# Kernel optimization log

Hardware: AMD Instinct MI355X
Metric: run time of the kernel (lower is better)

The kernel has to match this reference:

```python
import jax, jax.numpy as jnp
import numpy as np

N, E, IN_DIM, OUT_DIM, NTYPE, QDIM = 32, 512, 300, 300, 4, 300
SLOPE = 0.2  # lrelu:0.2


def setup_inputs() -> dict:
    key = jax.random.key(0)
    ks = jax.random.split(key, 8)
    return {
        "input_state": jax.random.normal(ks[0], (N, E, IN_DIM), jnp.float32),
        "adj": jax.random.randint(ks[1], (N, E, E), 0, NTYPE + 1, dtype=jnp.int32),
        "node_mask": jax.random.uniform(ks[2], (N, E, 1), jnp.float32),
        "query_vec": jax.random.normal(ks[3], (N, QDIM), jnp.float32),
        "W_type": jax.random.normal(ks[4], (NTYPE, IN_DIM, OUT_DIM), jnp.float32) * 0.02,
        "a_type": jax.random.normal(ks[5], (NTYPE, 2 * OUT_DIM), jnp.float32) * 0.02,
        "qattn_W1": jax.random.normal(ks[6], (NTYPE, QDIM, 2 * OUT_DIM), jnp.float32) * 0.02,
        "qattn_W2": jax.random.normal(ks[7], (NTYPE, 2 * OUT_DIM, 2 * OUT_DIM), jnp.float32) * 0.02,
    }


def reference(input_state, adj, node_mask, query_vec, W_type, a_type, qattn_W1, qattn_W2):
    # Faithful GAT head. The original builds an [N,E,E,2d] concat tensor; since
    # a_input[n,i,j] = [h_i, h_j] and the gate broadcasts over (i,j), the score
    # decomposes exactly as lrelu((h*g1)@a1 [:,i,None] + (h*g2)@a2 [:,None,j]).
    lrelu = lambda x: jnp.where(x >= 0, x, SLOPE * x)
    scores = jnp.zeros(adj.shape, jnp.float32)
    h = None
    for i in range(NTYPE):
        h = jnp.einsum("ned,df->nef", input_state, W_type[i])  # [N,E,d] (dropout: eval no-op)
        q_gate = jax.nn.relu(query_vec @ qattn_W1[i])
        q_gate = jax.nn.sigmoid(q_gate @ qattn_W2[i])          # [N,2d]
        g1, g2 = q_gate[:, :OUT_DIM], q_gate[:, OUT_DIM:]
        a1, a2 = a_type[i][:OUT_DIM], a_type[i][OUT_DIM:]
        s_src = jnp.einsum("ned,d->ne", h * g1[:, None, :], a1)  # contributes along i
        s_dst = jnp.einsum("ned,d->ne", h * g2[:, None, :], a2)  # contributes along j
        score = lrelu(s_src[:, :, None] + s_dst[:, None, :])      # [N,E,E]
        scores = scores + jnp.where(adj == i + 1, score, 0.0)
    scores = jnp.where(adj > 0, scores, jnp.float32(-1e30))
    h = h * node_mask  # note: original applies mask to h from the LAST edge type
    coefs = jax.nn.softmax(scores, axis=2)
    return jnp.einsum("nij,njd->nid", coefs, h)
```

## Files before the change

kernel.cpp:

```cpp
#include <hip/hip_runtime.h>
#include <hip/hip_bf16.h>

#define Nn   32
#define Ee   512
#define DIN  300
#define DOUT 300
#define NT   4
#define QD   300
#define SLOPE 0.2f
#define ROWS 64
#define CPAD 320
#define SSTR 516
#define USTR 65

typedef __attribute__((ext_vector_type(8))) short bf16x8;
typedef __attribute__((ext_vector_type(4))) float f32x4;
typedef __attribute__((ext_vector_type(4))) unsigned short u16x4;

__device__ inline unsigned short f2bf(float x) {
    __hip_bfloat16 h = __float2bfloat16(x);
    return *reinterpret_cast<unsigned short*>(&h);
}
__device__ inline float bf2f(unsigned short u) {
    __hip_bfloat16 h = *reinterpret_cast<__hip_bfloat16*>(&u);
    return __bfloat162float(h);
}
__device__ inline int swzj(int j) { return j ^ ((j >> 5) & 3); }

__global__ __launch_bounds__(256) void prep_kernel(
    const float* __restrict__ W3,
    unsigned short* __restrict__ W3T_hi,
    unsigned short* __restrict__ W3T_lo,
    unsigned short* __restrict__ UTh,
    unsigned short* __restrict__ UTl,
    unsigned short* __restrict__ GTh,
    unsigned short* __restrict__ GTl)
{
    int idx = blockIdx.x * 256 + threadIdx.x;
    if (idx < 320 * 320) {
        int c = idx / 320, k = idx - c * 320;
        float v = (c < DOUT && k < DIN) ? W3[(size_t)k * DOUT + c] : 0.f;
        unsigned short h = f2bf(v);
        W3T_hi[idx] = h;
        W3T_lo[idx] = f2bf(v - bf2f(h));
    }
    if (idx < 32 * 16 * 320) { UTh[idx] = 0; UTl[idx] = 0; }
    if (idx < 4 * 64 * 320)  { GTh[idx] = 0; GTl[idx] = 0; }
}

__global__ __launch_bounds__(256) void gates1_part_kernel(
    const float* __restrict__ q,
    const float* __restrict__ W1,
    float* __restrict__ t1p)
{
    int i = blockIdx.y, z = blockIdx.z;
    int idx = blockIdx.x * 256 + threadIdx.x;
    int n = idx / 600, j = idx - n * 600;
    const float* W1i = W1 + (size_t)i * QD * 600;
    const float* qn = q + n * QD;
    int k0 = z * 75;
    float a0 = 0.f;
    #pragma unroll 5
    for (int k = k0; k < k0 + 75; ++k)
        a0 += qn[k] * W1i[(size_t)k * 600 + j];
    t1p[((size_t)(z * NT + i) * Nn + n) * 600 + j] = a0;
}

__global__ __launch_bounds__(256) void gates1_fin_kernel(
    const float* __restrict__ t1p, float* __restrict__ t1)
{
    int i = blockIdx.y;
    int idx = blockIdx.x * 256 + threadIdx.x;
    size_t o = ((size_t)i * Nn) * 600 + idx;
    float s = t1p[o] + t1p[o + 76800] + t1p[o + 2 * 76800] + t1p[o + 3 * 76800];
    t1[o] = fmaxf(s, 0.f);
}

__global__ __launch_bounds__(256) void gates2_part_kernel(
    const float* __restrict__ t1,
    const float* __restrict__ W2,
    float* __restrict__ gp)
{
    int i = blockIdx.y, z = blockIdx.z;
    int idx = blockIdx.x * 256 + threadIdx.x;
    int n = idx / 600, j = idx - n * 600;
    const float* W2i = W2 + (size_t)i * 600 * 600;
    const float* tn = t1 + ((size_t)i * Nn + n) * 600;
    int k0 = z * 150;
    float a0 = 0.f, a1 = 0.f;
    #pragma unroll 5
    for (int k = k0; k < k0 + 150; k += 2) {
        a0 += tn[k]     * W2i[(size_t)k * 600 + j];
        a1 += tn[k + 1] * W2i[(size_t)(k + 1) * 600 + j];
    }
    gp[((size_t)(z * NT + i) * Nn + n) * 600 + j] = a0 + a1;
}

__global__ __launch_bounds__(256) void gates2_fin_kernel(
    const float* __restrict__ gp,
    const float* __restrict__ a,
    unsigned short* __restrict__ GTh,
    unsigned short* __restrict__ GTl)
{
    int i = blockIdx.y;
    int idx = blockIdx.x * 256 + threadIdx.x;
    int n = idx / 600, j = idx - n * 600;
    size_t o = ((size_t)i * Nn + n) * 600 + j;
    float s = gp[o] + gp[o + 76800] + gp[o + 2 * 76800] + gp[o + 3 * 76800];
    float w = (1.f / (1.f + __expf(-s))) * a[(size_t)i * 600 + j];
    int s2 = (j >= DOUT) ? 1 : 0;
    int d = j - s2 * DOUT;
    int c = 2 * n + s2;
    size_t go = ((size_t)i * 64 + c) * 320 + d;
    unsigned short h = f2bf(w);
    GTh[go] = h;
    GTl[go] = f2bf(w - bf2f(h));
}

__global__ __launch_bounds__(256) void uvec_mfma_kernel(
    const float* __restrict__ W,
    const unsigned short* __restrict__ GTh,
    const unsigned short* __restrict__ GTl,
    unsigned short* __restrict__ UTh,
    unsigned short* __restrict__ UTl)
{
    int mc = blockIdx.x, i = blockIdx.y;
    int tid = threadIdx.x, wv = tid >> 6, lane = tid & 63;
    int g = lane >> 4, cr = lane & 15;
    int m0 = mc * 64 + wv * 16;
    int arow = m0 + cr;
    const float* wr = W + (size_t)i * DIN * DOUT
                        + (size_t)(arow < DIN ? arow : 0) * DOUT;

    f32x4 acc[4];
    #pragma unroll
    for (int nt = 0; nt < 4; ++nt) acc[nt] = (f32x4){0.f, 0.f, 0.f, 0.f};

    for (int ks = 0; ks < 10; ++ks) {
        int k0 = ks * 32 + 8 * g;
        float x8[8];
        if (ks < 9) {
            f32x4 v0 = *(const f32x4*)(wr + k0);
            f32x4 v1 = *(const f32x4*)(wr + k0 + 4);
            #pragma unroll
            for (int j = 0; j < 4; ++j) { x8[j] = v0[j]; x8[4 + j] = v1[j]; }
        } else {
            #pragma unroll
            for (int j = 0; j < 8; ++j) {
                int d = k0 + j;
                x8[j] = (d < DOUT) ? wr[d] : 0.f;
            }
        }
        bf16x8 ahi, alo;
        #pragma unroll
        for (int j = 0; j < 8; ++j) {
            unsigned short h = f2bf(x8[j]);
            ahi[j] = (short)h;
            alo[j] = (short)f2bf(x8[j] - bf2f(h));
        }
        #pragma unroll
        for (int nt = 0; nt < 4; ++nt) {
            size_t bo = ((size_t)i * 64 + nt * 16 + cr) * 320 + k0;
            bf16x8 bh = *(const bf16x8*)(GTh + bo);
            bf16x8 bl = *(const bf16x8*)(GTl + bo);
            acc[nt] = __builtin_amdgcn_mfma_f32_16x16x32_bf16(ahi, bh, acc[nt], 0, 0, 0);
            acc[nt] = __builtin_amdgcn_mfma_f32_16x16x32_bf16(ahi, bl, acc[nt], 0, 0, 0);
            acc[nt] = __builtin_amdgcn_mfma_f32_16x16x32_bf16(alo, bh, acc[nt], 0, 0, 0);
        }
    }

    int krow = m0 + 4 * g;
    if (krow < DIN) {
        #pragma unroll
        for (int nt = 0; nt < 4; ++nt) {
            int c = nt * 16 + cr;
            int n = c >> 1, s = c & 1;
            size_t base = ((size_t)n * 16 + 2 * i + s) * 320 + krow;
            u16x4 h4, l4;
            #pragma unroll
            for (int q = 0; q < 4; ++q) {
                float v = acc[nt][q];
                unsigned short h = f2bf(v);
                h4[q] = h;
                l4[q] = f2bf(v - bf2f(h));
            }
            *(u16x4*)(UTh + base) = h4;
            *(u16x4*)(UTl + base) = l4;
        }
    }
}

__global__ __launch_bounds__(512) void hm_mfma_kernel(
    const float* __restrict__ X,
    const float* __restrict__ mask,
    const unsigned short* __restrict__ W3T_hi,
    const unsigned short* __restrict__ W3T_lo,
    const unsigned short* __restrict__ UTh,
    const unsigned short* __restrict__ UTl,
    unsigned short* __restrict__ hmT_hi,
    unsigned short* __restrict__ hmT_lo,
    float* __restrict__ ssrc,
    float* __restrict__ sdst)
{
    int tid = threadIdx.x, wv = tid >> 6, lane = tid & 63;
    int g = lane >> 4, cr = lane & 15;
    int f  = blockIdx.x;
    int n  = (f & 7) * 4 + ((f >> 3) & 3);
    int j0 = (f >> 5) * 64;
    size_t row0 = (size_t)n * Ee + j0;

    __shared__ float maskL[64];
    if (tid < 64) maskL[tid] = mask[row0 + tid];
    __syncthreads();

    f32x4 acc[3][4];
    f32x4 sacc[4];
    #pragma unroll
    for (int t = 0; t < 3; ++t)
        #pragma unroll
        for (int m = 0; m < 4; ++m) acc[t][m] = (f32x4){0.f, 0.f, 0.f, 0.f};
    #pragma unroll
    for (int m = 0; m < 4; ++m) sacc[m] = (f32x4){0.f, 0.f, 0.f, 0.f};

    const float* xr0 = X + (row0 +      cr) * DIN;
    const float* xr1 = X + (row0 + 16 + cr) * DIN;
    const float* xr2 = X + (row0 + 32 + cr) * DIN;
    const float* xr3 = X + (row0 + 48 + cr) * DIN;
    const float* xrs[4] = {xr0, xr1, xr2, xr3};

    for (int ks = 0; ks < 10; ++ks) {
        int k0 = ks * 32 + 8 * g;
        bf16x8 ahi[4], alo[4];
        #pragma unroll
        for (int m = 0; m < 4; ++m) {
            const float* xr = xrs[m];
            float x8[8];
            if (ks < 9) {
                f32x4 v0 = *(const f32x4*)(xr + k0);
                f32x4 v1 = *(const f32x4*)(xr + k0 + 4);
                #pragma unroll
                for (int j = 0; j < 4; ++j) { x8[j] = v0[j]; x8[4 + j] = v1[j]; }
            } else {
                #pragma unroll
                for (int j = 0; j < 8; ++j) {
                    int k = k0 + j;
                    x8[j] = (k < DIN) ? xr[k] : 0.f;
                }
            }
            #pragma unroll
            for (int j = 0; j < 8; ++j) {
                unsigned short h = f2bf(x8[j]);
                ahi[m][j] = (short)h;
                alo[m][j] = (short)f2bf(x8[j] - bf2f(h));
            }
        }
        #pragma unroll
        for (int t = 0; t < 3; ++t) {
            int ct = wv + 8 * t;
            if (ct < 19) {
                int c = ct * 16 + cr;
                bf16x8 bh = *(const bf16x8*)(W3T_hi + (size_t)c * 320 + k0);
                bf16x8 bl = *(const bf16x8*)(W3T_lo + (size_t)c * 320 + k0);
                #pragma unroll
                for (int m = 0; m < 4; ++m) {
                    acc[t][m] = __builtin_amdgcn_mfma_f32_16x16x32_bf16(ahi[m], bh, acc[t][m], 0, 0, 0);
                    acc[t][m] = __builtin_amdgcn_mfma_f32_16x16x32_bf16(ahi[m], bl, acc[t][m], 0, 0, 0);
                    acc[t][m] = __builtin_amdgcn_mfma_f32_16x16x32_bf16(alo[m], bh, acc[t][m], 0, 0, 0);
                }
            }
        }
        if (wv == 0) {
            bf16x8 uh = *(const bf16x8*)(UTh + ((size_t)n * 16 + cr) * 320 + k0);
            bf16x8 ul = *(const bf16x8*)(UTl + ((size_t)n * 16 + cr) * 320 + k0);
            #pragma unroll
            for (int m = 0; m < 4; ++m) {
                sacc[m] = __builtin_amdgcn_mfma_f32_16x16x32_bf16(ahi[m], uh, sacc[m], 0, 0, 0);
                sacc[m] = __builtin_amdgcn_mfma_f32_16x16x32_bf16(ahi[m], ul, sacc[m], 0, 0, 0);
                sacc[m] = __builtin_amdgcn_mfma_f32_16x16x32_bf16(alo[m], uh, sacc[m], 0, 0, 0);
            }
        }
    }

    #pragma unroll
    for (int t = 0; t < 3; ++t) {
        int ct = wv + 8 * t;
        if (ct < 19) {
            int c = ct * 16 + cr;
            #pragma unroll
            for (int m = 0; m < 4; ++m) {
                u16x4 h4, l4;
                #pragma unroll
                for (int qq = 0; qq < 4; ++qq) {
                    float v = acc[t][m][qq] * maskL[m * 16 + 4 * g + qq];
                    unsigned short h = f2bf(v);
                    h4[qq] = h;
                    l4[qq] = f2bf(v - bf2f(h));
                }
                size_t off = ((size_t)(n * CPAD + c)) * Ee + j0 + m * 16 + 4 * g;
                *(u16x4*)(hmT_hi + off) = h4;
                *(u16x4*)(hmT_lo + off) = l4;
            }
        }
    }

    if (wv == 0 && cr < 8) {
        int i = cr >> 1;
        float* dst = (cr & 1) ? sdst : ssrc;
        #pragma unroll
        for (int m = 0; m < 4; ++m)
            #pragma unroll
            for (int qq = 0; qq < 4; ++qq)
                dst[((size_t)i * Nn + n) * Ee + j0 + m * 16 + 4 * g + qq] = sacc[m][qq];
    }
}

__global__ __launch_bounds__(1024, 1) void attn64_kernel(
    const int*   __restrict__ adj,
    const float* __restrict__ ssrc,
    const float* __restrict__ sdst,
    const unsigned short* __restrict__ hmT_hi,
    const unsigned short* __restrict__ hmT_lo,
    float* __restrict__ out)
{
    int f  = blockIdx.x;
    int n  = (f & 7) * 4 + ((f >> 3) & 3);
    int rt = f >> 5;
    int tid = threadIdx.x;
    int row0 = rt * ROWS;

    __shared__ unsigned uni[Ee * USTR];
    __shared__ float sdl[NT * Ee];
    __shared__ float ssl[NT * 65];
    float* S = (float*)uni;

    for (int idx = tid; idx < NT * Ee; idx += 1024) {
        int i = idx >> 9, j = idx & (Ee - 1);
        sdl[i * Ee + swzj(j)] = sdst[((size_t)i * Nn + n) * Ee + j];
    }
    if (tid < NT * ROWS) {
        int i = tid >> 6, r = tid & 63;
        ssl[i * 65 + r] = ssrc[((size_t)i * Nn + n) * Ee + row0 + r];
    }
    __syncthreads();

    const int* adjb = adj + ((size_t)n * Ee + row0) * Ee;
    for (int idx4 = tid; idx4 < (ROWS * Ee) / 4; idx4 += 1024) {
        int r  = idx4 >> 7;
        int jb = (idx4 & 127) << 2;
        int xw = (jb >> 5) & 3;
        int4 t4 = *(const int4*)(adjb + (idx4 << 2));
        int tv[4] = {t4.x, t4.y, t4.z, t4.w};
        f32x4 v4;
        #pragma unroll
        for (int u = 0; u < 4; ++u) {
            int t = tv[u];
            float v;
            if (t > 0) {
                float x = ssl[(t - 1) * 65 + r] + sdl[(t - 1) * Ee + jb + (u ^ xw)];
                v = (x >= 0.f) ? x : SLOPE * x;
            } else {
                v = -1e30f;
            }
            v4[u] = v;
        }
        *(f32x4*)(S + r * SSTR + jb) = v4;
    }
    __syncthreads();

    int wv = tid >> 6, lane = tid & 63;
    float vals[4][8];
    float inv[4];
    #pragma unroll
    for (int rr = 0; rr < 4; ++rr) {
        int r = wv * 4 + rr;
        float m = -3.0e38f;
        #pragma unroll
        for (int k = 0; k < 8; ++k) {
            vals[rr][k] = S[r * SSTR + lane + 64 * k];
            m = fmaxf(m, vals[rr][k]);
        }
        #pragma unroll
        for (int off = 32; off; off >>= 1) m = fmaxf(m, __shfl_xor(m, off));
        float s = 0.f;
        #pragma unroll
        for (int k = 0; k < 8; ++k) {
            vals[rr][k] = __expf(vals[rr][k] - m);
            s += vals[rr][k];
        }
        #pragma unroll
        for (int off = 32; off; off >>= 1) s += __shfl_xor(s, off);
        inv[rr] = 1.f / s;
    }
    __syncthreads();

    #pragma unroll
    for (int rr = 0; rr < 4; ++rr) {
        int r = wv * 4 + rr;
        #pragma unroll
        for (int k = 0; k < 8; ++k) {
            float v = vals[rr][k] * inv[rr];
            unsigned short hi = f2bf(v);
            unsigned short lo = f2bf(v - bf2f(hi));
            uni[(lane + 64 * k) * USTR + r] = ((unsigned)hi << 16) | (unsigned)lo;
        }
    }
    __syncthreads();

    int g = lane >> 4, cr = lane & 15;
    f32x4 acc[2][4];
    #pragma unroll
    for (int t = 0; t < 2; ++t)
        #pragma unroll
        for (int m = 0; m < 4; ++m) acc[t][m] = (f32x4){0.f, 0.f, 0.f, 0.f};

#define LOADB(BH, BL, KS) do {                                              \
    int kk_ = (KS) * 32 + 8 * g;                                            \
    _Pragma("unroll")                                                       \
    for (int t_ = 0; t_ < 2; ++t_) {                                        \
        int ct_ = wv + 16 * t_;                                             \
        if (ct_ < 19) {                                                     \
            size_t off_ = ((size_t)(n * CPAD + ct_ * 16 + cr)) * Ee + kk_;  \
            BH[t_] = *(const bf16x8*)(hmT_hi + off_);                       \
            BL[t_] = *(const bf16x8*)(hmT_lo + off_);                       \
        }                                                                   \
    }                                                                       \
} while (0)

#define PVSTEP(KS, BH, BL) do {                                             \
    int kk_ = (KS) * 32;                                                    \
    bf16x8 ahi_[4], alo_[4];                                                \
    _Pragma("unroll")                                                       \
    for (int m_ = 0; m_ < 4; ++m_) {                                        \
        _Pragma("unroll")                                                   \
        for (int j_ = 0; j_ < 8; ++j_) {                                    \
            unsigned v_ = uni[(kk_ + 8 * g + j_) * USTR + m_ * 16 + cr];    \
            ahi_[m_][j_] = (short)(v_ >> 16);                               \
            alo_[m_][j_] = (short)(v_ & 0xffffu);                           \
        }                                                                   \
    }                                                                       \
    __builtin_amdgcn_s_setprio(1);                                          \
    _Pragma("unroll")                                                       \
    for (int t_ = 0; t_ < 2; ++t_) {                                        \
        if (wv + 16 * t_ < 19) {                                            \
            _Pragma("unroll")                                               \
            for (int m_ = 0; m_ < 4; ++m_) {                                \
                acc[t_][m_] = __builtin_amdgcn_mfma_f32_16x16x32_bf16(ahi_[m_], BH[t_], acc[t_][m_], 0, 0, 0); \
                acc[t_][m_] = __builtin_amdgcn_mfma_f32_16x16x32_bf16(ahi_[m_], BL[t_], acc[t_][m_], 0, 0, 0); \
                acc[t_][m_] = __builtin_amdgcn_mfma_f32_16x16x32_bf16(alo_[m_], BH[t_], acc[t_][m_], 0, 0, 0); \
            }                                                               \
        }                                                                   \
    }                                                                       \
    __builtin_amdgcn_s_setprio(0);                                          \
} while (0)

    bf16x8 bhA[2], blA[2], bhB[2], blB[2];
    LOADB(bhA, blA, 0);
    #pragma unroll
    for (int ks = 0; ks < 16; ks += 2) {
        LOADB(bhB, blB, ks + 1);
        PVSTEP(ks, bhA, blA);
        if (ks + 2 < 16) LOADB(bhA, blA, ks + 2);
        PVSTEP(ks + 1, bhB, blB);
    }
#undef LOADB
#undef PVSTEP

    #pragma unroll
    for (int t = 0; t < 2; ++t) {
        int ct = wv + 16 * t;
        if (ct < 19) {
            int c = ct * 16 + cr;
            if (c < DOUT) {
                #pragma unroll
                for (int m = 0; m < 4; ++m) {
                    #pragma unroll
                    for (int q = 0; q < 4; ++q) {
                        int erow = row0 + m * 16 + 4 * g + q;
                        out[((size_t)n * Ee + erow) * DOUT + c] = acc[t][m][q];
                    }
                }
            }
        }
    }
}

extern "C" void kernel_launch(void* const* d_in, const int* in_sizes, int n_in,
                              void* d_out, int out_size, void* d_ws, size_t ws_size,
                              hipStream_t stream) {
    const float* input_state = (const float*)d_in[0];
    const int*   adj         = (const int*)  d_in[1];
    const float* node_mask   = (const float*)d_in[2];
    const float* query_vec   = (const float*)d_in[3];
    const float* W_type      = (const float*)d_in[4];
    const float* a_type      = (const float*)d_in[5];
    const float* qattn_W1    = (const float*)d_in[6];
    const float* qattn_W2    = (const float*)d_in[7];
    float* out = (float*)d_out;

    float* ws   = (float*)d_ws;
    float* t1   = ws;
    float* ssrc = t1   + 76800;
    float* sdst = ssrc + 65536;
    unsigned short* W3T_hi = (unsigned short*)(sdst + 65536);
    unsigned short* W3T_lo = W3T_hi + 320 * 320;
    unsigned short* GTh    = W3T_lo + 320 * 320;
    unsigned short* GTl    = GTh + 4 * 64 * 320;
    unsigned short* UTh    = GTl + 4 * 64 * 320;
    unsigned short* UTl    = UTh + 32 * 16 * 320;
    unsigned short* hmT_hi = UTl + 32 * 16 * 320;
    unsigned short* hmT_lo = hmT_hi + (size_t)Nn * CPAD * Ee;
    float* t1p = (float*)(hmT_lo + (size_t)Nn * CPAD * Ee);
    float* gp  = t1p + 307200;

    hipLaunchKernelGGL(prep_kernel, dim3(640), dim3(256), 0, stream,
                       W_type + 3 * DIN * DOUT, W3T_hi, W3T_lo, UTh, UTl, GTh, GTl);
    hipLaunchKernelGGL(gates1_part_kernel, dim3(75, NT, 4), dim3(256), 0, stream,
                       query_vec, qattn_W1, t1p);
    hipLaunchKernelGGL(gates1_fin_kernel, dim3(75, NT), dim3(256), 0, stream,
                       t1p, t1);
    hipLaunchKernelGGL(gates2_part_kernel, dim3(75, NT, 4), dim3(256), 0, stream,
                       t1, qattn_W2, gp);
    hipLaunchKernelGGL(gates2_fin_kernel, dim3(75, NT), dim3(256), 0, stream,
                       gp, a_type, GTh, GTl);
    hipLaunchKernelGGL(uvec_mfma_kernel, dim3(5, NT), dim3(256), 0, stream,
                       W_type, GTh, GTl, UTh, UTl);
    hipLaunchKernelGGL(hm_mfma_kernel, dim3((Nn * Ee) / 64), dim3(512), 0, stream,
                       input_state, node_mask, W3T_hi, W3T_lo, UTh, UTl,
                       hmT_hi, hmT_lo, ssrc, sdst);
    hipLaunchKernelGGL(attn64_kernel, dim3(256), dim3(1024), 0, stream,
                       adj, ssrc, sdst, hmT_hi, hmT_lo, out);
}
```

Baseline: 114.4 us.

## Fuse gate prep kernels to cut launches from eight to five

Merges the weight-transpose prep with the first gate partial GEMM into one launch, and folds the first split-K reduction plus ReLU into the second gate GEMM's inner loop. The second reduction, the sigmoid and the multiply by the attention vector move into the uvec kernel, which now builds the gate matrix in shared memory instead of reading it from global. This removes three launches and their intermediate global round-trips. In exchange, each gate-2 thread re-reads four partial sums per k, and every uvec block recomputes the sigmoid gate tile redundantly.

```diff
diff --git a/kernel.cpp b/kernel.cpp
--- a/kernel.cpp
+++ b/kernel.cpp
@@ -12,6 +12,7 @@
 #define CPAD 320
 #define SSTR 516
 #define USTR 65
+#define GSTR 328
 
 typedef __attribute__((ext_vector_type(8))) short bf16x8;
 typedef __attribute__((ext_vector_type(4))) float f32x4;
@@ -27,57 +28,47 @@
 }
 __device__ inline int swzj(int j) { return j ^ ((j >> 5) & 3); }
 
-__global__ __launch_bounds__(256) void prep_kernel(
+__global__ __launch_bounds__(256) void prep_g1_kernel(
     const float* __restrict__ W3,
+    const float* __restrict__ q,
+    const float* __restrict__ W1,
     unsigned short* __restrict__ W3T_hi,
     unsigned short* __restrict__ W3T_lo,
     unsigned short* __restrict__ UTh,
     unsigned short* __restrict__ UTl,
-    unsigned short* __restrict__ GTh,
-    unsigned short* __restrict__ GTl)
-{
-    int idx = blockIdx.x * 256 + threadIdx.x;
-    if (idx < 320 * 320) {
-        int c = idx / 320, k = idx - c * 320;
-        float v = (c < DOUT && k < DIN) ? W3[(size_t)k * DOUT + c] : 0.f;
-        unsigned short h = f2bf(v);
-        W3T_hi[idx] = h;
-        W3T_lo[idx] = f2bf(v - bf2f(h));
-    }
-    if (idx < 32 * 16 * 320) { UTh[idx] = 0; UTl[idx] = 0; }
-    if (idx < 4 * 64 * 320)  { GTh[idx] = 0; GTl[idx] = 0; }
-}
-
-__global__ __launch_bounds__(256) void gates1_part_kernel(
-    const float* __restrict__ q,
-    const float* __restrict__ W1,
     float* __restrict__ t1p)
 {
-    int i = blockIdx.y, z = blockIdx.z;
-    int idx = blockIdx.x * 256 + threadIdx.x;
-    int n = idx / 600, j = idx - n * 600;
-    const float* W1i = W1 + (size_t)i * QD * 600;
-    const float* qn = q + n * QD;
-    int k0 = z * 75;
-    float a0 = 0.f;
-    #pragma unroll 5
-    for (int k = k0; k < k0 + 75; ++k)
-        a0 += qn[k] * W1i[(size_t)k * 600 + j];
-    t1p[((size_t)(z * NT + i) * Nn + n) * 600 + j] = a0;
-}
-
-__global__ __launch_bounds__(256) void gates1_fin_kernel(
-    const float* __restrict__ t1p, float* __restrict__ t1)
-{
-    int i = blockIdx.y;
-    int idx = blockIdx.x * 256 + threadIdx.x;
-    size_t o = ((size_t)i * Nn) * 600 + idx;
-    float s = t1p[o] + t1p[o + 76800] + t1p[o + 2 * 76800] + t1p[o + 3 * 76800];
-    t1[o] = fmaxf(s, 0.f);
+    int b = blockIdx.x, tid = threadIdx.x;
+    if (b < 640) {
+        int idx = b * 256 + tid;
+        if (idx < 320 * 320) {
+            int c = idx / 320, k = idx - c * 320;
+            float v = (c < DOUT && k < DIN) ? W3[(size_t)k * DOUT + c] : 0.f;
+            unsigned short h = f2bf(v);
+            W3T_hi[idx] = h;
+            W3T_lo[idx] = f2bf(v - bf2f(h));
+        }
+        if (idx < 32 * 16 * 320) { UTh[idx] = 0; UTl[idx] = 0; }
+    } else {
+        int bb = b - 640;
+        int jt = bb % 75;
+        int rest = bb / 75;
+        int i = rest & 3, z = rest >> 2;
+        int idx = jt * 256 + tid;
+        int n = idx / 600, j = idx - n * 600;
+        const float* W1i = W1 + (size_t)i * QD * 600;
+        const float* qn = q + n * QD;
+        int k0 = z * 75;
+        float a0 = 0.f;
+        #pragma unroll 5
+        for (int k = k0; k < k0 + 75; ++k)
+            a0 += qn[k] * W1i[(size_t)k * 600 + j];
+        t1p[((size_t)(z * NT + i) * Nn + n) * 600 + j] = a0;
+    }
 }
 
 __global__ __launch_bounds__(256) void gates2_part_kernel(
-    const float* __restrict__ t1,
+    const float* __restrict__ t1p,
     const float* __restrict__ W2,
     float* __restrict__ gp)
 {
@@ -85,48 +76,48 @@
     int idx = blockIdx.x * 256 + threadIdx.x;
     int n = idx / 600, j = idx - n * 600;
     const float* W2i = W2 + (size_t)i * 600 * 600;
-    const float* tn = t1 + ((size_t)i * Nn + n) * 600;
+    const float* tb = t1p + ((size_t)i * Nn + n) * 600;
     int k0 = z * 150;
     float a0 = 0.f, a1 = 0.f;
     #pragma unroll 5
     for (int k = k0; k < k0 + 150; k += 2) {
-        a0 += tn[k]     * W2i[(size_t)k * 600 + j];
-        a1 += tn[k + 1] * W2i[(size_t)(k + 1) * 600 + j];
+        float tv0 = fmaxf(tb[k]     + tb[k + 76800]     + tb[k + 153600]     + tb[k + 230400],     0.f);
+        float tv1 = fmaxf(tb[k + 1] + tb[k + 1 + 76800] + tb[k + 1 + 153600] + tb[k + 1 + 230400], 0.f);
+        a0 += tv0 * W2i[(size_t)k * 600 + j];
+        a1 += tv1 * W2i[(size_t)(k + 1) * 600 + j];
     }
     gp[((size_t)(z * NT + i) * Nn + n) * 600 + j] = a0 + a1;
 }
 
-__global__ __launch_bounds__(256) void gates2_fin_kernel(
+__global__ __launch_bounds__(256) void uvec2_kernel(
+    const float* __restrict__ W,
     const float* __restrict__ gp,
     const float* __restrict__ a,
-    unsigned short* __restrict__ GTh,
-    unsigned short* __restrict__ GTl)
-{
-    int i = blockIdx.y;
-    int idx = blockIdx.x * 256 + threadIdx.x;
-    int n = idx / 600, j = idx - n * 600;
-    size_t o = ((size_t)i * Nn + n) * 600 + j;
-    float s = gp[o] + gp[o + 76800] + gp[o + 2 * 76800] + gp[o + 3 * 76800];
-    float w = (1.f / (1.f + __expf(-s))) * a[(size_t)i * 600 + j];
-    int s2 = (j >= DOUT) ? 1 : 0;
-    int d = j - s2 * DOUT;
-    int c = 2 * n + s2;
-    size_t go = ((size_t)i * 64 + c) * 320 + d;
-    unsigned short h = f2bf(w);
-    GTh[go] = h;
-    GTl[go] = f2bf(w - bf2f(h));
-}
-
-__global__ __launch_bounds__(256) void uvec_mfma_kernel(
-    const float* __restrict__ W,
-    const unsigned short* __restrict__ GTh,
-    const unsigned short* __restrict__ GTl,
     unsigned short* __restrict__ UTh,
     unsigned short* __restrict__ UTl)
 {
     int mc = blockIdx.x, i = blockIdx.y;
     int tid = threadIdx.x, wv = tid >> 6, lane = tid & 63;
     int g = lane >> 4, cr = lane & 15;
+
+    __shared__ unsigned short GTsh[64 * GSTR];
+    __shared__ unsigned short GTsl[64 * GSTR];
+
+    for (int idx = tid; idx < 64 * GSTR; idx += 256) {
+        int c = idx / GSTR, d = idx - c * GSTR;
+        float w = 0.f;
+        if (d < DOUT) {
+            int n = c >> 1, s = c & 1;
+            size_t o = ((size_t)i * Nn + n) * 600 + s * DOUT + d;
+            float sum = gp[o] + gp[o + 76800] + gp[o + 153600] + gp[o + 230400];
+            w = (1.f / (1.f + __expf(-sum))) * a[(size_t)i * 600 + s * DOUT + d];
+        }
+        unsigned short h = f2bf(w);
+        GTsh[idx] = h;
+        GTsl[idx] = f2bf(w - bf2f(h));
+    }
+    __syncthreads();
+
     int m0 = mc * 64 + wv * 16;
     int arow = m0 + cr;
     const float* wr = W + (size_t)i * DIN * DOUT
@@ -160,9 +151,9 @@
         }
         #pragma unroll
         for (int nt = 0; nt < 4; ++nt) {
-            size_t bo = ((size_t)i * 64 + nt * 16 + cr) * 320 + k0;
-            bf16x8 bh = *(const bf16x8*)(GTh + bo);
-            bf16x8 bl = *(const bf16x8*)(GTl + bo);
+            int bo = (nt * 16 + cr) * GSTR + k0;
+            bf16x8 bh = *(const bf16x8*)(GTsh + bo);
+            bf16x8 bl = *(const bf16x8*)(GTsl + bo);
             acc[nt] = __builtin_amdgcn_mfma_f32_16x16x32_bf16(ahi, bh, acc[nt], 0, 0, 0);
             acc[nt] = __builtin_amdgcn_mfma_f32_16x16x32_bf16(ahi, bl, acc[nt], 0, 0, 0);
             acc[nt] = __builtin_amdgcn_mfma_f32_16x16x32_bf16(alo, bh, acc[nt], 0, 0, 0);
@@ -511,19 +502,15 @@
     unsigned short* hmT_lo = hmT_hi + (size_t)Nn * CPAD * Ee;
     float* t1p = (float*)(hmT_lo + (size_t)Nn * CPAD * Ee);
     float* gp  = t1p + 307200;
-
-    hipLaunchKernelGGL(prep_kernel, dim3(640), dim3(256), 0, stream,
-                       W_type + 3 * DIN * DOUT, W3T_hi, W3T_lo, UTh, UTl, GTh, GTl);
-    hipLaunchKernelGGL(gates1_part_kernel, dim3(75, NT, 4), dim3(256), 0, stream,
-                       query_vec, qattn_W1, t1p);
-    hipLaunchKernelGGL(gates1_fin_kernel, dim3(75, NT), dim3(256), 0, stream,
-                       t1p, t1);
+    (void)GTh; (void)GTl;
+
+    hipLaunchKernelGGL(prep_g1_kernel, dim3(1840), dim3(256), 0, stream,
+                       W_type + 3 * DIN * DOUT, query_vec, qattn_W1,
+                       W3T_hi, W3T_lo, UTh, UTl, t1p);
     hipLaunchKernelGGL(gates2_part_kernel, dim3(75, NT, 4), dim3(256), 0, stream,
-                       t1, qattn_W2, gp);
-    hipLaunchKernelGGL(gates2_fin_kernel, dim3(75, NT), dim3(256), 0, stream,
-                       gp, a_type, GTh, GTl);
-    hipLaunchKernelGGL(uvec_mfma_kernel, dim3(5, NT), dim3(256), 0, stream,
-                       W_type, GTh, GTl, UTh, UTl);
+                       t1p, qattn_W2, gp);
+    hipLaunchKernelGGL(uvec2_kernel, dim3(5, NT), dim3(256), 0, stream,
+                       W_type, gp, a_type, UTh, UTl);
     hipLaunchKernelGGL(hm_mfma_kernel, dim3((Nn * Ee) / 64), dim3(512), 0, stream,
                        input_state, node_mask, W3T_hi, W3T_lo, UTh, UTl,
                        hmT_hi, hmT_lo, ssrc, sdst);
```

New measurement: 154.1 us. +34.7%, slower.
